# Kernel tuning notes

Measured on AMD Instinct MI355X. Metric: run time of the kernel, lower is better.

The kernel has to match this reference:

```python
import jax, jax.numpy as jnp
import numpy as np

D = 192      # d_model
DE = 96      # d_edge
H = 8        # n_heads
DH = D // H  # d_head = 24
DF = 2 * D   # ff hidden = 384
N = 25000
E = 400000


def _layernorm(x, s, b, eps=1e-5):
    m = jnp.mean(x, axis=-1, keepdims=True)
    v = jnp.var(x, axis=-1, keepdims=True)
    return (x - m) * jax.lax.rsqrt(v + eps) * s + b


def setup_inputs() -> dict:
    key = jax.random.key(0)
    ks = jax.random.split(key, 12)
    sc = lambda d: 1.0 / np.sqrt(d)
    inp = {
        "x": jax.random.normal(ks[0], (N, D), jnp.float32),
        "edge_feat": jax.random.normal(ks[1], (E, DE), jnp.float32),
        "edge_index": jax.random.randint(ks[2], (2, E), 0, N, jnp.int64),
        # attention projections (stored [d_in, d_out], applied as x @ W)
        "Wq": jax.random.normal(ks[3], (D, D), jnp.float32) * sc(D),
        "Wk": jax.random.normal(ks[4], (D, D), jnp.float32) * sc(D),
        "Wv": jax.random.normal(ks[5], (D, D), jnp.float32) * sc(D),
        "We": jax.random.normal(ks[6], (DE, H), jnp.float32) * sc(DE),
        "Wo": jax.random.normal(ks[7], (D, D), jnp.float32) * sc(D),
        "bo": jnp.zeros((D,), jnp.float32),
        "Wg": jax.random.normal(ks[8], (2 * D, D), jnp.float32) * sc(2 * D),
        "bg": jnp.zeros((D,), jnp.float32),
        "ln1_s": jnp.ones((D,), jnp.float32),
        "ln1_b": jnp.zeros((D,), jnp.float32),
        "Wf1": jax.random.normal(ks[9], (D, DF), jnp.float32) * sc(D),
        "bf1": jnp.zeros((DF,), jnp.float32),
        "Wf2": jax.random.normal(ks[10], (DF, D), jnp.float32) * sc(DF),
        "bf2": jnp.zeros((D,), jnp.float32),
        "ln2_s": jnp.ones((D,), jnp.float32),
        "ln2_b": jnp.zeros((D,), jnp.float32),
    }
    return inp


def reference(x, edge_feat, edge_index, Wq, Wk, Wv, We, Wo, bo, Wg, bg,
              ln1_s, ln1_b, Wf1, bf1, Wf2, bf2, ln2_s, ln2_b):
    src, dst = edge_index[0], edge_index[1]
    n = x.shape[0]
    # per-edge gathered projections: [E, H, DH]
    q = (x[dst] @ Wq).reshape(-1, H, DH)
    k = (x[src] @ Wk).reshape(-1, H, DH)
    v = (x[src] @ Wv).reshape(-1, H, DH)
    score = jnp.sum(q * k, axis=-1) / np.sqrt(DH) + edge_feat @ We  # [E, H]
    # segment softmax over incoming edges of each dst node
    mx = jax.ops.segment_max(score, dst, num_segments=n)           # [N, H]
    alpha = jnp.exp(score - mx[dst])                                # [E, H]
    den = jax.ops.segment_sum(alpha, dst, num_segments=n)          # [N, H]
    num = jax.ops.segment_sum(alpha[..., None] * v, dst, num_segments=n)  # [N, H, DH]
    agg = (num / (den[:, :, None] + 1e-8)).reshape(n, D)
    o = agg @ Wo + bo
    g = jax.nn.sigmoid(jnp.concatenate([o, x], axis=-1) @ Wg + bg)
    y = _layernorm(g * o + (1.0 - g) * x, ln1_s, ln1_b)
    ff = jax.nn.silu(y @ Wf1 + bf1) @ Wf2 + bf2
    return _layernorm(y + ff, ln2_s, ln2_b)
```

## Files before the change

### kernel.cpp

```cpp
#include <hip/hip_runtime.h>
#include <cstdint>
#include <cstddef>

#define LOG2E 1.4426950408889634f

constexpr int Dm  = 192;
constexpr int DEe = 96;

typedef unsigned short u16;
typedef __attribute__((ext_vector_type(8))) short short8v;
typedef __attribute__((ext_vector_type(4))) float f32x4;
typedef __attribute__((ext_vector_type(4))) uint32_t u32x4;

__device__ __forceinline__ u16 f2bf(float f) {
    uint32_t u = __builtin_bit_cast(uint32_t, f);
    uint32_t r = (u + 0x7FFF + ((u >> 16) & 1)) >> 16;
    return (u16)r;
}
__device__ __forceinline__ float bf2f(u16 h) {
    uint32_t u = ((uint32_t)h) << 16;
    return __builtin_bit_cast(float, u);
}
__device__ __forceinline__ uint32_t cvtpk_bf16(float lo, float hi) {
    uint32_t r;
    asm("v_cvt_pk_bf16_f32 %0, %1, %2" : "=v"(r) : "v"(lo), "v"(hi));
    return r;
}

__global__ void zero_ints(int* __restrict__ p, int n) {
    int i = blockIdx.x * blockDim.x + threadIdx.x;
    if (i < n) p[i] = 0;
}

__global__ __launch_bounds__(1024) void scan_kernel(const int* __restrict__ deg, int N,
                                                    int* __restrict__ offs) {
    __shared__ int sp[1024];
    int t = threadIdx.x;
    int per = (N + 1023) >> 10;
    int base = t * per;
    int sum = 0;
    for (int i = 0; i < per; ++i) {
        int idx = base + i;
        if (idx < N) sum += deg[idx];
    }
    sp[t] = sum;
    __syncthreads();
    for (int off = 1; off < 1024; off <<= 1) {
        int v = (t >= off) ? sp[t - off] : 0;
        __syncthreads();
        sp[t] += v;
        __syncthreads();
    }
    int run = sp[t] - sum;
    for (int i = 0; i < per; ++i) {
        int idx = base + i;
        if (idx < N) { offs[idx] = run; run += deg[idx]; }
    }
    if (t == 1023) offs[N] = sp[1023];
}

__global__ __launch_bounds__(256) void prepA(
    const int* __restrict__ ei, int E,
    const float* __restrict__ x, int n4, u16* __restrict__ xb,
    const float* __restrict__ Wq, const float* __restrict__ Wk,
    const float* __restrict__ Wv, const float* __restrict__ Wo,
    const float* __restrict__ Wg, const float* __restrict__ Wf1,
    const float* __restrict__ Wf2, const float* __restrict__ We,
    u16* __restrict__ Wqkvt, u16* __restrict__ Wot,
    u16* __restrict__ Wgt, u16* __restrict__ Wf1t, u16* __restrict__ Wf2t,
    u16* __restrict__ Wet,
    int* __restrict__ deg)
{
    int i = blockIdx.x * 256 + threadIdx.x;
    if (i < E) {
        atomicAdd(&deg[ei[E + i]], 1);
        return;
    }
    i -= E;
    if (i < n4) {
        float4 v = ((const float4*)x)[i];
        uint32_t p0 = cvtpk_bf16(v.x, v.y);
        uint32_t p1 = cvtpk_bf16(v.z, v.w);
        ushort4 o;
        o.x = (u16)(p0 & 0xffff); o.y = (u16)(p0 >> 16);
        o.z = (u16)(p1 & 0xffff); o.w = (u16)(p1 >> 16);
        ((ushort4*)xb)[i] = o;
        return;
    }
    int idx = i - n4;
    if (idx < 110592) {
        int n = idx / 192, k = idx % 192;
        const float* W = n < 192 ? Wq : (n < 384 ? Wk : Wv);
        Wqkvt[idx] = f2bf(W[(size_t)k * 192 + (n % 192)]);
    } else if (idx < 147456) {
        int j = idx - 110592;
        int n = j / 192, k = j % 192;
        Wot[j] = f2bf(Wo[(size_t)k * 192 + n]);
    } else if (idx < 221184) {
        int j = idx - 147456;
        int n = j / 384, k = j % 384;
        Wgt[j] = f2bf(Wg[(size_t)k * 192 + n]);
    } else if (idx < 294912) {
        int j = idx - 221184;
        int n = j / 192, k = j % 192;
        Wf1t[j] = f2bf(Wf1[(size_t)k * 384 + n]);
    } else if (idx < 368640) {
        int j = idx - 294912;
        int n = j / 384, k = j % 384;
        Wf2t[j] = f2bf(Wf2[(size_t)k * 192 + n]);
    } else if (idx < 370176) {
        int j = idx - 368640;
        int n = j / 96, k = j % 96;
        Wet[j] = (n < 8) ? f2bf(We[(size_t)k * 8 + n] * LOG2E) : (u16)0;
    }
}

__global__ __launch_bounds__(256) void phaseC(
    int EB,
    int E, const float* __restrict__ ef, const u16* __restrict__ Wet,
    float* __restrict__ esb,
    const u16* __restrict__ xb, int M, int gm64,
    const u16* __restrict__ Wt, u16* __restrict__ qkvb)
{
    int bid = blockIdx.x;
    int tid = threadIdx.x;
    int w = tid >> 6, lane = tid & 63;
    int c16 = lane & 15, hi2 = lane >> 4, kof = hi2 * 8;

    if (bid < EB) {
        int ebase = bid * 256 + w * 64;
        if (ebase >= E) return;

        short8v bfr[3];
        #pragma unroll
        for (int ks = 0; ks < 3; ++ks)
            bfr[ks] = *(const short8v*)(Wet + (size_t)c16 * 96 + ks * 32 + kof);

        #pragma unroll 1
        for (int mt = 0; mt < 4; ++mt) {
            int er = ebase + mt * 16 + c16;
            if (er > E - 1) er = E - 1;
            const float* efr = ef + (size_t)er * 96;

            f32x4 acc = (f32x4)(0.f);
            #pragma unroll
            for (int ks = 0; ks < 3; ++ks) {
                float4 fa = *(const float4*)(efr + ks * 32 + kof);
                float4 fb = *(const float4*)(efr + ks * 32 + kof + 4);
                u32x4 pk;
                pk.x = cvtpk_bf16(fa.x, fa.y);
                pk.y = cvtpk_bf16(fa.z, fa.w);
                pk.z = cvtpk_bf16(fb.x, fb.y);
                pk.w = cvtpk_bf16(fb.z, fb.w);
                short8v af = __builtin_bit_cast(short8v, pk);
                acc = __builtin_amdgcn_mfma_f32_16x16x32_bf16(af, bfr[ks], acc, 0, 0, 0);
            }

            int erow0 = ebase + mt * 16 + hi2 * 4;
            #pragma unroll
            for (int reg = 0; reg < 4; ++reg) {
                int e = erow0 + reg;
                if (e < E && c16 < 8)
                    esb[(size_t)e * 8 + c16] = acc[reg];
            }
        }
        return;
    }

    int qb = bid - EB;
    int m0 = (qb % gm64) * 64, n0 = (qb / gm64) * 192;

    int rcm[4];
    #pragma unroll
    for (int mr = 0; mr < 4; ++mr) {
        int r = m0 + mr * 16 + c16;
        rcm[mr] = r < M ? r : M - 1;
    }

    f32x4 acc[4][3];
    #pragma unroll
    for (int mr = 0; mr < 4; ++mr)
        #pragma unroll
        for (int nr = 0; nr < 3; ++nr) acc[mr][nr] = (f32x4)(0.f);

    #pragma unroll 1
    for (int ks = 0; ks < 6; ++ks) {
        short8v af[4], bfr[3];
        #pragma unroll
        for (int mr = 0; mr < 4; ++mr)
            af[mr] = *(const short8v*)(xb + (size_t)rcm[mr] * 192 + ks * 32 + kof);
        #pragma unroll
        for (int nr = 0; nr < 3; ++nr)
            bfr[nr] = *(const short8v*)(Wt + (size_t)(n0 + w * 48 + nr * 16 + c16) * 192 + ks * 32 + kof);
        #pragma unroll
        for (int mr = 0; mr < 4; ++mr)
            #pragma unroll
            for (int nr = 0; nr < 3; ++nr)
                acc[mr][nr] = __builtin_amdgcn_mfma_f32_16x16x32_bf16(
                    af[mr], bfr[nr], acc[mr][nr], 0, 0, 0);
    }

    #pragma unroll
    for (int mr = 0; mr < 4; ++mr)
        #pragma unroll
        for (int nr = 0; nr < 3; ++nr) {
            uint32_t p0 = cvtpk_bf16(acc[mr][nr][0], acc[mr][nr][1]);
            uint32_t p1 = cvtpk_bf16(acc[mr][nr][2], acc[mr][nr][3]);
            int r0 = m0 + mr * 16 + hi2 * 4;
            int col = n0 + w * 48 + nr * 16 + c16;
            if (r0     < M) qkvb[(size_t)(r0    ) * 576 + col] = (u16)(p0 & 0xffff);
            if (r0 + 1 < M) qkvb[(size_t)(r0 + 1) * 576 + col] = (u16)(p0 >> 16);
            if (r0 + 2 < M) qkvb[(size_t)(r0 + 2) * 576 + col] = (u16)(p1 & 0xffff);
            if (r0 + 3 < M) qkvb[(size_t)(r0 + 3) * 576 + col] = (u16)(p1 >> 16);
        }
}

__global__ __launch_bounds__(256) void scatter_k(
    const int* __restrict__ ei, int E,
    const float* __restrict__ esb,
    const int* __restrict__ offs, int* __restrict__ cur,
    float* __restrict__ scb, int* __restrict__ sbuf)
{
    int e = blockIdx.x * 256 + threadIdx.x;
    if (e >= E) return;
    float4 a = ((const float4*)esb)[(size_t)e * 2];
    float4 b = ((const float4*)esb)[(size_t)e * 2 + 1];
    int src = ei[e];
    int dst = ei[E + e];
    int pos = offs[dst] + atomicAdd(&cur[dst], 1);
    sbuf[pos] = src;
    ((float4*)scb)[(size_t)pos * 2]     = a;
    ((float4*)scb)[(size_t)pos * 2 + 1] = b;
}

__global__ __launch_bounds__(256) void agg_fused(
    const u16* __restrict__ qkv, const float* __restrict__ scb,
    const int* __restrict__ sbuf, const int* __restrict__ offs,
    int N, u16* __restrict__ aggb)
{
    int node = blockIdx.x * 4 + (threadIdx.x >> 6);
    if (node >= N) return;
    int lane = threadIdx.x & 63;
    int h = lane >> 3;
    int di = (3 * lane) >> 1;
    int odd = lane & 1;

    int beg = offs[node], end = offs[node + 1];
    u16* og = aggb + (size_t)node * Dm;
    int b0 = 3 * lane;
    if (beg >= end) {
        og[b0] = 0; og[b0 + 1] = 0; og[b0 + 2] = 0;
        return;
    }

    const uint32_t* qrow = (const uint32_t*)(qkv + (size_t)node * 576);
    uint32_t qd0 = qrow[di], qd1 = qrow[di + 1];
    float q0, q1, q2;
    if (!odd) { q0 = bf2f(qd0 & 0xffff); q1 = bf2f(qd0 >> 16); q2 = bf2f(qd1 & 0xffff); }
    else      { q0 = bf2f(qd0 >> 16);    q1 = bf2f(qd1 & 0xffff); q2 = bf2f(qd1 >> 16); }

    auto clampi = [&](int i) { return i < end ? i : end - 1; };

    float den = 0.f, a0 = 0.f, a1 = 0.f, a2 = 0.f;

    uint32_t ck[2][2], cv[2][2]; float cep[2];
    uint32_t nk[2][2], nv[2][2]; float nep[2];
    int s0, s1;

    {
        int p00 = clampi(beg),     p01 = clampi(beg + 1);
        int p10 = clampi(beg + 2), p11 = clampi(beg + 3);
        int sA = sbuf[p00], sB = sbuf[p01], sC = sbuf[p10], sD = sbuf[p11];
        const uint32_t* r;
        r = (const uint32_t*)(qkv + (size_t)sA * 576 + 192);
        ck[0][0] = r[di]; ck[0][1] = r[di + 1];
        r = (const uint32_t*)(qkv + (size_t)sA * 576 + 384);
        cv[0][0] = r[di]; cv[0][1] = r[di + 1];
        r = (const uint32_t*)(qkv + (size_t)sB * 576 + 192);
        ck[1][0] = r[di]; ck[1][1] = r[di + 1];
        r = (const uint32_t*)(qkv + (size_t)sB * 576 + 384);
        cv[1][0] = r[di]; cv[1][1] = r[di + 1];
        r = (const uint32_t*)(qkv + (size_t)sC * 576 + 192);
        nk[0][0] = r[di]; nk[0][1] = r[di + 1];
        r = (const uint32_t*)(qkv + (size_t)sC * 576 + 384);
        nv[0][0] = r[di]; nv[0][1] = r[di + 1];
        r = (const uint32_t*)(qkv + (size_t)sD * 576 + 192);
        nk[1][0] = r[di]; nk[1][1] = r[di + 1];
        r = (const uint32_t*)(qkv + (size_t)sD * 576 + 384);
        nv[1][0] = r[di]; nv[1][1] = r[di + 1];
        cep[0] = scb[(size_t)p00 * 8 + h]; cep[1] = scb[(size_t)p01 * 8 + h];
        nep[0] = scb[(size_t)p10 * 8 + h]; nep[1] = scb[(size_t)p11 * 8 + h];
        s0 = sbuf[clampi(beg + 4)]; s1 = sbuf[clampi(beg + 5)];
    }

    for (int idx = beg; idx < end; idx += 2) {
        #pragma unroll
        for (int j = 0; j < 2; ++j) {
            float k0, k1, k2, v0, v1, v2;
            uint32_t kd0 = ck[j][0], kd1 = ck[j][1];
            uint32_t vd0 = cv[j][0], vd1 = cv[j][1];
            if (!odd) {
                k0 = bf2f(kd0 & 0xffff); k1 = bf2f(kd0 >> 16); k2 = bf2f(kd1 & 0xffff);
                v0 = bf2f(vd0 & 0xffff); v1 = bf2f(vd0 >> 16); v2 = bf2f(vd1 & 0xffff);
            } else {
                k0 = bf2f(kd0 >> 16); k1 = bf2f(kd1 & 0xffff); k2 = bf2f(kd1 >> 16);
                v0 = bf2f(vd0 >> 16); v1 = bf2f(vd1 & 0xffff); v2 = bf2f(vd1 >> 16);
            }
            float pd = q0 * k0 + q1 * k1 + q2 * k2;
            pd += __shfl_xor(pd, 1, 64);
            pd += __shfl_xor(pd, 2, 64);
            pd += __shfl_xor(pd, 4, 64);
            float p = exp2f(pd * 0.2944885836f + cep[j]);
            if (idx + j < end) {
                den += p;
                a0 += p * v0; a1 += p * v1; a2 += p * v2;
            }
        }
        #pragma unroll
        for (int j = 0; j < 2; ++j) {
            ck[j][0] = nk[j][0]; ck[j][1] = nk[j][1];
            cv[j][0] = nv[j][0]; cv[j][1] = nv[j][1];
            cep[j] = nep[j];
        }
        {
            const uint32_t* r;
            r = (const uint32_t*)(qkv + (size_t)s0 * 576 + 192);
            nk[0][0] = r[di]; nk[0][1] = r[di + 1];
            r = (const uint32_t*)(qkv + (size_t)s0 * 576 + 384);
            nv[0][0] = r[di]; nv[0][1] = r[di + 1];
            r = (const uint32_t*)(qkv + (size_t)s1 * 576 + 192);
            nk[1][0] = r[di]; nk[1][1] = r[di + 1];
            r = (const uint32_t*)(qkv + (size_t)s1 * 576 + 384);
            nv[1][0] = r[di]; nv[1][1] = r[di + 1];
            nep[0] = scb[(size_t)clampi(idx + 4) * 8 + h];
            nep[1] = scb[(size_t)clampi(idx + 5) * 8 + h];
        }
        s0 = sbuf[clampi(idx + 6)]; s1 = sbuf[clampi(idx + 7)];
    }

    float rden = 1.f / (den + 1e-8f);
    og[b0]     = f2bf(a0 * rden);
    og[b0 + 1] = f2bf(a1 * rden);
    og[b0 + 2] = f2bf(a2 * rden);
}

__global__ __launch_bounds__(512) void chain_fused(
    const u16* __restrict__ aggb, const u16* __restrict__ xb, int M,
    const u16* __restrict__ Wot, const float* __restrict__ bo,
    const u16* __restrict__ Wgt, const float* __restrict__ bg,
    const float* __restrict__ l1s, const float* __restrict__ l1b,
    const u16* __restrict__ Wf1t, const float* __restrict__ bf1,
    const u16* __restrict__ Wf2t, const float* __restrict__ bf2,
    const float* __restrict__ l2s, const float* __restrict__ l2b,
    float* __restrict__ out)
{
    __shared__ __align__(16) short Ybuf[128 * 200];
    __shared__ __align__(16) short Fbuf[128 * 392];
    __shared__ float red[2][4][128];

    int tid = threadIdx.x;
    int m0 = blockIdx.x * 128;
    int w = tid >> 6, lane = tid & 63;
    int wr = w >> 2, wc = w & 3;
    int c16 = lane & 15, hi2 = lane >> 4, kof = hi2 * 8;
    int rbase = m0 + wr * 64;
    int lbase = wr * 64;

    int rcm[4];
    #pragma unroll
    for (int mr = 0; mr < 4; ++mr) {
        int r = rbase + mr * 16 + c16;
        rcm[mr] = r < M ? r : M - 1;
    }

    f32x4 oacc[4][3];
    #pragma unroll
    for (int mr = 0; mr < 4; ++mr)
        #pragma unroll
        for (int nr = 0; nr < 3; ++nr) oacc[mr][nr] = (f32x4)(0.f);
    #pragma unroll 1
    for (int ks = 0; ks < 6; ++ks) {
        short8v af[4], bfr[3];
        #pragma unroll
        for (int mr = 0; mr < 4; ++mr)
            af[mr] = *(const short8v*)(aggb + (size_t)rcm[mr] * 192 + ks * 32 + kof);
        #pragma unroll
        for (int nr = 0; nr < 3; ++nr)
            bfr[nr] = *(const short8v*)(Wot + (size_t)(wc * 48 + nr * 16 + c16) * 192 + ks * 32 + kof);
        #pragma unroll
        for (int mr = 0; mr < 4; ++mr)
            #pragma unroll
            for (int nr = 0; nr < 3; ++nr)
                oacc[mr][nr] = __builtin_amdgcn_mfma_f32_16x16x32_bf16(
                    af[mr], bfr[nr], oacc[mr][nr], 0, 0, 0);
    }
    #pragma unroll
    for (int nr = 0; nr < 3; ++nr) {
        int col = wc * 48 + nr * 16 + c16;
        float b = bo[col];
        #pragma unroll
        for (int mr = 0; mr < 4; ++mr) {
            #pragma unroll
            for (int reg = 0; reg < 4; ++reg) oacc[mr][nr][reg] += b;
            uint32_t p0 = cvtpk_bf16(oacc[mr][nr][0], oacc[mr][nr][1]);
            uint32_t p1 = cvtpk_bf16(oacc[mr][nr][2], oacc[mr][nr][3]);
            int row0 = lbase + mr * 16 + hi2 * 4;
            Ybuf[(row0    ) * 200 + col] = (short)(p0 & 0xffff);
            Ybuf[(row0 + 1) * 200 + col] = (short)(p0 >> 16);
            Ybuf[(row0 + 2) * 200 + col] = (short)(p1 & 0xffff);
            Ybuf[(row0 + 3) * 200 + col] = (short)(p1 >> 16);
        }
    }
    __syncthreads();

    f32x4 zacc[4][3];
    #pragma unroll
    for (int mr = 0; mr < 4; ++mr)
        #pragma unroll
        for (int nr = 0; nr < 3; ++nr) zacc[mr][nr] = (f32x4)(0.f);
    #pragma unroll 1
    for (int ks = 0; ks < 6; ++ks) {
        short8v af[4], bfr[3];
        #pragma unroll
        for (int mr = 0; mr < 4; ++mr)
            af[mr] = *(const short8v*)&Ybuf[(lbase + mr * 16 + c16) * 200 + ks * 32 + kof];
        #pragma unroll
        for (int nr = 0; nr < 3; ++nr)
            bfr[nr] = *(const short8v*)(Wgt + (size_t)(wc * 48 + nr * 16 + c16) * 384 + ks * 32 + kof);
        #pragma unroll
        for (int mr = 0; mr < 4; ++mr)
            #pragma unroll
            for (int nr = 0; nr < 3; ++nr)
                zacc[mr][nr] = __builtin_amdgcn_mfma_f32_16x16x32_bf16(
                    af[mr], bfr[nr], zacc[mr][nr], 0, 0, 0);
    }
    #pragma unroll 1
    for (int ks = 0; ks < 6; ++ks) {
        short8v af[4], bfr[3];
        #pragma unroll
        for (int mr = 0; mr < 4; ++mr)
            af[mr] = *(const short8v*)(xb + (size_t)rcm[mr] * 192 + ks * 32 + kof);
        #pragma unroll
        for (int nr = 0; nr < 3; ++nr)
            bfr[nr] = *(const short8v*)(Wgt + (size_t)(wc * 48 + nr * 16 + c16) * 384 + 192 + ks * 32 + kof);
        #pragma unroll
        for (int mr = 0; mr < 4; ++mr)
            #pragma unroll
            for (int nr = 0; nr < 3; ++nr)
                zacc[mr][nr] = __builtin_amdgcn_mfma_f32_16x16x32_bf16(
                    af[mr], bfr[nr], zacc[mr][nr], 0, 0, 0);
    }
    float s1p[4][4], s2p[4][4];
    #pragma unroll
    for (int mr = 0; mr < 4; ++mr)
        #pragma unroll
        for (int reg = 0; reg < 4; ++reg) {
            int gr = rbase + mr * 16 + hi2 * 4 + reg;
            int rcR = gr < M ? gr : M - 1;
            float s1 = 0.f, s2 = 0.f;
            #pragma unroll
            for (int nr = 0; nr < 3; ++nr) {
                int col = wc * 48 + nr * 16 + c16;
                float z = zacc[mr][nr][reg] + bg[col];
                float g = 1.f / (1.f + expf(-z));
                float xv = bf2f(xb[(size_t)rcR * 192 + col]);
                float val = g * oacc[mr][nr][reg] + (1.f - g) * xv;
                zacc[mr][nr][reg] = val;
                s1 += val; s2 += val * val;
            }
            #pragma unroll
            for (int mS = 1; mS < 16; mS <<= 1) {
                s1 += __shfl_xor(s1, mS, 64);
                s2 += __shfl_xor(s2, mS, 64);
            }
            s1p[mr][reg] = s1; s2p[mr][reg] = s2;
        }
    if (c16 == 0) {
        #pragma unroll
        for (int mr = 0; mr < 4; ++mr)
            #pragma unroll
            for (int reg = 0; reg < 4; ++reg) {
                int rowIdx = lbase + mr * 16 + hi2 * 4 + reg;
                red[0][wc][rowIdx] = s1p[mr][reg];
                red[1][wc][rowIdx] = s2p[mr][reg];
            }
    }
    __syncthreads();
    #pragma unroll
    for (int mr = 0; mr < 4; ++mr)
        #pragma unroll
        for (int reg = 0; reg < 4; ++reg) {
            int rowIdx = lbase + mr * 16 + hi2 * 4 + reg;
            float S1 = red[0][0][rowIdx] + red[0][1][rowIdx] + red[0][2][rowIdx] + red[0][3][rowIdx];
            float S2 = red[1][0][rowIdx] + red[1][1][rowIdx] + red[1][2][rowIdx] + red[1][3][rowIdx];
            float mean = S1 * (1.f / 192.f);
            float var  = S2 * (1.f / 192.f) - mean * mean;
            float inv  = rsqrtf(var + 1e-5f);
            #pragma unroll
            for (int nr = 0; nr < 3; ++nr) {
                int col = wc * 48 + nr * 16 + c16;
                float yv = (zacc[mr][nr][reg] - mean) * inv * l1s[col] + l1b[col];
                Ybuf[rowIdx * 200 + col] = (short)f2bf(yv);
            }
        }
    __syncthreads();

    f32x4 tacc[4][6];
    #pragma unroll
    for (int mr = 0; mr < 4; ++mr)
        #pragma unroll
        for (int nr = 0; nr < 6; ++nr) tacc[mr][nr] = (f32x4)(0.f);
    #pragma unroll 1
    for (int ks = 0; ks < 6; ++ks) {
        short8v af[4], bfr[6];
        #pragma unroll
        for (int mr = 0; mr < 4; ++mr)
            af[mr] = *(const short8v*)&Ybuf[(lbase + mr * 16 + c16) * 200 + ks * 32 + kof];
        #pragma unroll
        for (int nr = 0; nr < 6; ++nr)
            bfr[nr] = *(const short8v*)(Wf1t + (size_t)(wc * 96 + nr * 16 + c16) * 192 + ks * 32 + kof);
        #pragma unroll
        for (int mr = 0; mr < 4; ++mr)
            #pragma unroll
            for (int nr = 0; nr < 6; ++nr)
                tacc[mr][nr] = __builtin_amdgcn_mfma_f32_16x16x32_bf16(
                    af[mr], bfr[nr], tacc[mr][nr], 0, 0, 0);
    }
    #pragma unroll
    for (int nr = 0; nr < 6; ++nr) {
        int col = wc * 96 + nr * 16 + c16;
        float b = bf1[col];
        #pragma unroll
        for (int mr = 0; mr < 4; ++mr) {
            float t0[4];
            #pragma unroll
            for (int reg = 0; reg < 4; ++reg) {
                float z = tacc[mr][nr][reg] + b;
                t0[reg] = z / (1.f + expf(-z));
            }
            uint32_t p0 = cvtpk_bf16(t0[0], t0[1]);
            uint32_t p1 = cvtpk_bf16(t0[2], t0[3]);
            int row0 = lbase + mr * 16 + hi2 * 4;
            Fbuf[(row0    ) * 392 + col] = (short)(p0 & 0xffff);
            Fbuf[(row0 + 1) * 392 + col] = (short)(p0 >> 16);
            Fbuf[(row0 + 2) * 392 + col] = (short)(p1 & 0xffff);
            Fbuf[(row0 + 3) * 392 + col] = (short)(p1 >> 16);
        }
    }
    __syncthreads();

    f32x4 facc[4][3];
    #pragma unroll
    for (int mr = 0; mr < 4; ++mr)
        #pragma unroll
        for (int nr = 0; nr < 3; ++nr) facc[mr][nr] = (f32x4)(0.f);
    #pragma unroll 1
    for (int ks = 0; ks < 12; ++ks) {
        short8v af[4], bfr[3];
        #pragma unroll
        for (int mr = 0; mr < 4; ++mr)
            af[mr] = *(const short8v*)&Fbuf[(lbase + mr * 16 + c16) * 392 + ks * 32 + kof];
        #pragma unroll
        for (int nr = 0; nr < 3; ++nr)
            bfr[nr] = *(const short8v*)(Wf2t + (size_t)(wc * 48 + nr * 16 + c16) * 384 + ks * 32 + kof);
        #pragma unroll
        for (int mr = 0; mr < 4; ++mr)
            #pragma unroll
            for (int nr = 0; nr < 3; ++nr)
                facc[mr][nr] = __builtin_amdgcn_mfma_f32_16x16x32_bf16(
                    af[mr], bfr[nr], facc[mr][nr], 0, 0, 0);
    }
    float s1q[4][4], s2q[4][4];
    #pragma unroll
    for (int mr = 0; mr < 4; ++mr)
        #pragma unroll
        for (int reg = 0; reg < 4; ++reg) {
            int rowIdx = lbase + mr * 16 + hi2 * 4 + reg;
            float s1 = 0.f, s2 = 0.f;
            #pragma unroll
            for (int nr = 0; nr < 3; ++nr) {
                int col = wc * 48 + nr * 16 + c16;
                float val = facc[mr][nr][reg] + bf2[col] + bf2f((u16)Ybuf[rowIdx * 200 + col]);
                facc[mr][nr][reg] = val;
                s1 += val; s2 += val * val;
            }
            #pragma unroll
            for (int mS = 1; mS < 16; mS <<= 1) {
                s1 += __shfl_xor(s1, mS, 64);
                s2 += __shfl_xor(s2, mS, 64);
            }
            s1q[mr][reg] = s1; s2q[mr][reg] = s2;
        }
    if (c16 == 0) {
        #pragma unroll
        for (int mr = 0; mr < 4; ++mr)
            #pragma unroll
            for (int reg = 0; reg < 4; ++reg) {
                int rowIdx = lbase + mr * 16 + hi2 * 4 + reg;
                red[0][wc][rowIdx] = s1q[mr][reg];
                red[1][wc][rowIdx] = s2q[mr][reg];
            }
    }
    __syncthreads();
    #pragma unroll
    for (int mr = 0; mr < 4; ++mr)
        #pragma unroll
        for (int reg = 0; reg < 4; ++reg) {
            int rowIdx = lbase + mr * 16 + hi2 * 4 + reg;
            int r = m0 + rowIdx;
            if (r >= M) continue;
            float S1 = red[0][0][rowIdx] + red[0][1][rowIdx] + red[0][2][rowIdx] + red[0][3][rowIdx];
            float S2 = red[1][0][rowIdx] + red[1][1][rowIdx] + red[1][2][rowIdx] + red[1][3][rowIdx];
            float mean = S1 * (1.f / 192.f);
            float var  = S2 * (1.f / 192.f) - mean * mean;
            float inv  = rsqrtf(var + 1e-5f);
            #pragma unroll
            for (int nr = 0; nr < 3; ++nr) {
                int col = wc * 48 + nr * 16 + c16;
                out[(size_t)r * 192 + col] =
                    (facc[mr][nr][reg] - mean) * inv * l2s[col] + l2b[col];
            }
        }
}

extern "C" void kernel_launch(void* const* d_in, const int* in_sizes, int n_in,
                              void* d_out, int out_size, void* d_ws, size_t ws_size,
                              hipStream_t stream) {
    const float* x   = (const float*)d_in[0];
    const float* ef  = (const float*)d_in[1];
    const int*   ei  = (const int*)d_in[2];
    const float* Wq  = (const float*)d_in[3];
    const float* Wk  = (const float*)d_in[4];
    const float* Wv  = (const float*)d_in[5];
    const float* We  = (const float*)d_in[6];
    const float* Wo  = (const float*)d_in[7];
    const float* bo  = (const float*)d_in[8];
    const float* Wg  = (const float*)d_in[9];
    const float* bg  = (const float*)d_in[10];
    const float* l1s = (const float*)d_in[11];
    const float* l1b = (const float*)d_in[12];
    const float* Wf1 = (const float*)d_in[13];
    const float* bf1 = (const float*)d_in[14];
    const float* Wf2 = (const float*)d_in[15];
    const float* bf2 = (const float*)d_in[16];
    const float* l2s = (const float*)d_in[17];
    const float* l2b = (const float*)d_in[18];

    int N = in_sizes[0] / Dm;
    int E = in_sizes[1] / DEe;
    float* out = (float*)d_out;

    char* wp = (char*)d_ws;
    auto alloc = [&](size_t bytes) -> void* {
        void* p = wp;
        wp += (bytes + 255) & ~(size_t)255;
        return p;
    };
    size_t NF = (size_t)N * Dm;
    u16*   xb     = (u16*)alloc(NF * 2);
    u16*   qkvb   = (u16*)alloc((size_t)N * 576 * 2);
    u16*   aggb   = (u16*)alloc(NF * 2);
    float* scb    = (float*)alloc((size_t)E * 8 * 4);
    float* esb    = (float*)alloc((size_t)E * 8 * 4);
    int*   sbuf   = (int*)  alloc((size_t)E * 4);
    int*   degcur = (int*)  alloc((size_t)2 * N * 4);
    int*   offs   = (int*)  alloc((size_t)(N + 1) * 4);
    u16*   Wqkvt  = (u16*)alloc((size_t)576 * 192 * 2);
    u16*   Wot    = (u16*)alloc((size_t)192 * 192 * 2);
    u16*   Wgt    = (u16*)alloc((size_t)192 * 384 * 2);
    u16*   Wf1t   = (u16*)alloc((size_t)384 * 192 * 2);
    u16*   Wf2t   = (u16*)alloc((size_t)192 * 384 * 2);
    u16*   Wet    = (u16*)alloc((size_t)16 * 96 * 2);
    int* deg = degcur;
    int* cur = degcur + N;

    int gm64  = (N + 63) / 64;
    int gm128 = (N + 127) / 128;
    int n4 = N * Dm / 4;

    zero_ints<<<dim3((2 * N + 255) / 256), 256, 0, stream>>>(degcur, 2 * N);

    int prepTotal = E + n4 + 370176;
    prepA<<<dim3((prepTotal + 255) / 256), 256, 0, stream>>>(
        ei, E, x, n4, xb, Wq, Wk, Wv, Wo, Wg, Wf1, Wf2, We,
        Wqkvt, Wot, Wgt, Wf1t, Wf2t, Wet, deg);

    scan_kernel<<<dim3(1), 1024, 0, stream>>>(deg, N, offs);

    int EB = (E + 255) / 256;
    int QB = gm64 * 3;
    phaseC<<<dim3(EB + QB), 256, 0, stream>>>(EB,
        E, ef, Wet, esb,
        xb, N, gm64, Wqkvt, qkvb);

    scatter_k<<<dim3(EB), 256, 0, stream>>>(ei, E, esb, offs, cur, scb, sbuf);

    agg_fused<<<dim3((N + 3) / 4), 256, 0, stream>>>(qkvb, scb, sbuf, offs, N, aggb);

    chain_fused<<<dim3(gm128), 512, 0, stream>>>(aggb, xb, N,
        Wot, bo, Wgt, bg, l1s, l1b, Wf1t, bf1, Wf2t, bf2, l2s, l2b, out);
}
```

Measured before the change: 273.7 us.

## Compute CSR positions before edge-score GEMM and scatter scores directly

A new kernel computes each edge's CSR position (and the source list) before phaseC, so the edge-score MFMA can write its scores straight into the dst-sorted buffer. This removes the intermediate esb buffer and its extra read/write pass. phaseC's edge path also now stages each 64-edge tile of edge features through shared memory with coalesced float4 loads, using one 16-row tile per wave. The trade-off is an extra int pos array round trip, scattered 4-byte score writes instead of float4 writes, and a 25.6 KB shared allocation that also applies to the QKV GEMM blocks and may reduce their occupancy.

```diff
diff --git a/kernel.cpp b/kernel.cpp
--- a/kernel.cpp
+++ b/kernel.cpp
@@ -115,53 +115,73 @@
     }
 }
 
+__global__ __launch_bounds__(256) void posk(
+    const int* __restrict__ ei, int E,
+    const int* __restrict__ offs, int* __restrict__ cur,
+    int* __restrict__ pos, int* __restrict__ sbuf)
+{
+    int e = blockIdx.x * 256 + threadIdx.x;
+    if (e >= E) return;
+    int src = ei[e];
+    int dst = ei[E + e];
+    int p = offs[dst] + atomicAdd(&cur[dst], 1);
+    pos[e] = p;
+    sbuf[p] = src;
+}
+
 __global__ __launch_bounds__(256) void phaseC(
     int EB,
     int E, const float* __restrict__ ef, const u16* __restrict__ Wet,
-    float* __restrict__ esb,
+    const int* __restrict__ pos, float* __restrict__ scb,
     const u16* __restrict__ xb, int M, int gm64,
     const u16* __restrict__ Wt, u16* __restrict__ qkvb)
 {
+    __shared__ float efs[64 * 100];
+
     int bid = blockIdx.x;
     int tid = threadIdx.x;
     int w = tid >> 6, lane = tid & 63;
     int c16 = lane & 15, hi2 = lane >> 4, kof = hi2 * 8;
 
     if (bid < EB) {
-        int ebase = bid * 256 + w * 64;
-        if (ebase >= E) return;
+        int ebase = bid * 64;
+        #pragma unroll
+        for (int rep = 0; rep < 6; ++rep) {
+            int idx = tid + 256 * rep;
+            int row = idx / 24, c4 = idx % 24;
+            int g = ebase + row; if (g > E - 1) g = E - 1;
+            float4 v = *(const float4*)(ef + (size_t)g * 96 + c4 * 4);
+            *(float4*)&efs[row * 100 + c4 * 4] = v;
+        }
+        __syncthreads();
 
         short8v bfr[3];
         #pragma unroll
         for (int ks = 0; ks < 3; ++ks)
             bfr[ks] = *(const short8v*)(Wet + (size_t)c16 * 96 + ks * 32 + kof);
 
-        #pragma unroll 1
-        for (int mt = 0; mt < 4; ++mt) {
-            int er = ebase + mt * 16 + c16;
-            if (er > E - 1) er = E - 1;
-            const float* efr = ef + (size_t)er * 96;
-
-            f32x4 acc = (f32x4)(0.f);
-            #pragma unroll
-            for (int ks = 0; ks < 3; ++ks) {
-                float4 fa = *(const float4*)(efr + ks * 32 + kof);
-                float4 fb = *(const float4*)(efr + ks * 32 + kof + 4);
-                u32x4 pk;
-                pk.x = cvtpk_bf16(fa.x, fa.y);
-                pk.y = cvtpk_bf16(fa.z, fa.w);
-                pk.z = cvtpk_bf16(fb.x, fb.y);
-                pk.w = cvtpk_bf16(fb.z, fb.w);
-                short8v af = __builtin_bit_cast(short8v, pk);
-                acc = __builtin_amdgcn_mfma_f32_16x16x32_bf16(af, bfr[ks], acc, 0, 0, 0);
-            }
-
-            int erow0 = ebase + mt * 16 + hi2 * 4;
-            #pragma unroll
-            for (int reg = 0; reg < 4; ++reg) {
-                int e = erow0 + reg;
-                if (e < E && c16 < 8)
-                    esb[(size_t)e * 8 + c16] = acc[reg];
+        int lrow = w * 16 + c16;
+        f32x4 acc = (f32x4)(0.f);
+        #pragma unroll
+        for (int ks = 0; ks < 3; ++ks) {
+            float4 fa = *(const float4*)&efs[lrow * 100 + ks * 32 + kof];
+            float4 fb = *(const float4*)&efs[lrow * 100 + ks * 32 + kof + 4];
+            u32x4 pk;
+            pk.x = cvtpk_bf16(fa.x, fa.y);
+            pk.y = cvtpk_bf16(fa.z, fa.w);
+            pk.z = cvtpk_bf16(fb.x, fb.y);
+            pk.w = cvtpk_bf16(fb.z, fb.w);
+            short8v af = __builtin_bit_cast(short8v, pk);
+            acc = __builtin_amdgcn_mfma_f32_16x16x32_bf16(af, bfr[ks], acc, 0, 0, 0);
+        }
+
+        int erow0 = ebase + w * 16 + hi2 * 4;
+        #pragma unroll
+        for (int reg = 0; reg < 4; ++reg) {
+            int e = erow0 + reg;
+            if (e < E && c16 < 8) {
+                int p = pos[e];
+                scb[(size_t)p * 8 + c16] = acc[reg];
             }
         }
         return;
@@ -213,24 +233,6 @@
             if (r0 + 2 < M) qkvb[(size_t)(r0 + 2) * 576 + col] = (u16)(p1 & 0xffff);
             if (r0 + 3 < M) qkvb[(size_t)(r0 + 3) * 576 + col] = (u16)(p1 >> 16);
         }
-}
-
-__global__ __launch_bounds__(256) void scatter_k(
-    const int* __restrict__ ei, int E,
-    const float* __restrict__ esb,
-    const int* __restrict__ offs, int* __restrict__ cur,
-    float* __restrict__ scb, int* __restrict__ sbuf)
-{
-    int e = blockIdx.x * 256 + threadIdx.x;
-    if (e >= E) return;
-    float4 a = ((const float4*)esb)[(size_t)e * 2];
-    float4 b = ((const float4*)esb)[(size_t)e * 2 + 1];
-    int src = ei[e];
-    int dst = ei[E + e];
-    int pos = offs[dst] + atomicAdd(&cur[dst], 1);
-    sbuf[pos] = src;
-    ((float4*)scb)[(size_t)pos * 2]     = a;
-    ((float4*)scb)[(size_t)pos * 2 + 1] = b;
 }
 
 __global__ __launch_bounds__(256) void agg_fused(
@@ -661,7 +663,7 @@
     u16*   qkvb   = (u16*)alloc((size_t)N * 576 * 2);
     u16*   aggb   = (u16*)alloc(NF * 2);
     float* scb    = (float*)alloc((size_t)E * 8 * 4);
-    float* esb    = (float*)alloc((size_t)E * 8 * 4);
+    int*   pos    = (int*)  alloc((size_t)E * 4);
     int*   sbuf   = (int*)  alloc((size_t)E * 4);
     int*   degcur = (int*)  alloc((size_t)2 * N * 4);
     int*   offs   = (int*)  alloc((size_t)(N + 1) * 4);
@@ -687,13 +689,13 @@
 
     scan_kernel<<<dim3(1), 1024, 0, stream>>>(deg, N, offs);
 
-    int EB = (E + 255) / 256;
+    posk<<<dim3((E + 255) / 256), 256, 0, stream>>>(ei, E, offs, cur, pos, sbuf);
+
+    int EB = (E + 63) / 64;
     int QB = gm64 * 3;
     phaseC<<<dim3(EB + QB), 256, 0, stream>>>(EB,
-        E, ef, Wet, esb,
+        E, ef, Wet, pos, scb,
         xb, N, gm64, Wqkvt, qkvb);
-
-    scatter_k<<<dim3(EB), 256, 0, stream>>>(ei, E, esb, offs, cur, scb, sbuf);
 
     agg_fused<<<dim3((N + 3) / 4), 256, 0, stream>>>(qkvb, scb, sbuf, offs, N, aggb);
 
```

Result: no change. 270.1 us (-1.3%).
